# Kernel tuning notes

Measured on AMD Instinct MI355X. Metric: run time of the kernel, lower is better.

Reference implementation:

```python
import jax, jax.numpy as jnp
import numpy as np

D_MODEL = 1024


def pos_encoding(seq_len, d_model):
    # pos: [S,1], i: [d/2]
    pos = jnp.arange(seq_len, dtype=jnp.float32)[:, None]
    i = jnp.arange(0, d_model, 2, dtype=jnp.float32)
    angle_rates = 1.0 / jnp.power(10000.0, i / d_model)
    angle_rads = pos * angle_rates  # [S, d/2]
    # NOTE: original concatenates sin block then cos block (not interleaved)
    return jnp.concatenate([jnp.sin(angle_rads), jnp.cos(angle_rads)], axis=-1)  # [S, d]


def setup_inputs() -> dict:
    key = jax.random.key(0)
    ks = jax.random.split(key, 4)
    B, S, D = 4, 2048, D_MODEL
    scale = 1.0 / np.sqrt(D)
    x = jax.random.normal(ks[0], (B, S, D), dtype=jnp.float32)
    Wq = jax.random.normal(ks[1], (D, D), dtype=jnp.float32) * scale
    Wk = jax.random.normal(ks[2], (D, D), dtype=jnp.float32) * scale
    Wv = jax.random.normal(ks[3], (D, D), dtype=jnp.float32) * scale
    bq = jnp.zeros((D,), dtype=jnp.float32)
    bk = jnp.zeros((D,), dtype=jnp.float32)
    bv = jnp.zeros((D,), dtype=jnp.float32)
    return {"x": x, "Wq": Wq, "bq": bq, "Wk": Wk, "bk": bk, "Wv": Wv, "bv": bv}


def reference(x, Wq, bq, Wk, bk, Wv, bv):
    B, S, D = x.shape
    pe = pos_encoding(S, D)  # [S, D]
    h = x + pe[None, :, :]
    q = jnp.einsum('bsd,de->bse', h, Wq) + bq
    k = jnp.einsum('bsd,de->bse', h, Wk) + bk
    v = jnp.einsum('bsd,de->bse', h, Wv) + bv
    logits = jnp.einsum('bqd,bkd->bqk', q, k) / jnp.sqrt(jnp.float32(D))
    attn = jax.nn.softmax(logits, axis=-1)
    out = jnp.einsum('bqk,bkd->bqd', attn, v)
    return x + out
```

## Files before the change

kernel.cpp:

```cpp
#include <hip/hip_runtime.h>
#include <stdint.h>


#define AS1(p) ((__attribute__((address_space(1))) void*)(p))
#define AS3(p) ((__attribute__((address_space(3))) void*)(p))

typedef _Float16 f16x8 __attribute__((ext_vector_type(8)));
typedef _Float16 f16x4 __attribute__((ext_vector_type(4)));
typedef float f32x4 __attribute__((ext_vector_type(4)));

__global__ __launch_bounds__(256) void prep(const float* __restrict__ x,
                                            _Float16* __restrict__ h,
                                            const float* __restrict__ Wq,
                                            const float* __restrict__ Wk,
                                            const float* __restrict__ Wv,
                                            _Float16* __restrict__ Wt,
                                            float* __restrict__ rowsum) {
  const int bx = blockIdx.x;
  const int tid = threadIdx.x;
  if (bx < 8192) {
    const size_t e = ((size_t)bx * 256 + tid) * 4;
    const int d = (int)(e & 1023);
    const int s = (int)((e >> 10) & 2047);
    const float4 xv = *(const float4*)(x + e);
    const int half = d >> 9;
    const int j0 = d & 511;
    const float c = -0.017988946039016f;
    f16x4 o;
#pragma unroll
    for (int t = 0; t < 4; t++) {
      const float r = __expf((float)(j0 + t) * c);
      const float a = (float)s * r;
      const float p = half ? __cosf(a) : __sinf(a);
      const float xe = (t == 0) ? xv.x : (t == 1) ? xv.y : (t == 2) ? xv.z : xv.w;
      o[t] = (_Float16)(xe + p);
    }
    *(f16x4*)(h + e) = o;
  } else if (bx < 11264) {
    __shared__ float t[32][33];
    const int w = bx - 8192;
    const int z = w >> 10;
    const int rem = w & 1023;
    const int n0 = (rem & 31) * 32, k0 = (rem >> 5) * 32;
    const float* W = (z == 0) ? Wq : (z == 1) ? Wk : Wv;
    _Float16* o = Wt + (size_t)z * 1048576;
    const int tx = tid & 31, ty = tid >> 5;
#pragma unroll
    for (int i = ty; i < 32; i += 8)
      t[i][tx] = W[(size_t)(k0 + i) * 1024 + (n0 + tx)];
    __syncthreads();
#pragma unroll
    for (int i = ty; i < 32; i += 8)
      o[(size_t)(n0 + i) * 1024 + (k0 + tx)] = (_Float16)t[tx][i];
  } else {
    rowsum[(bx - 11264) * 256 + tid] = 0.f;
  }
}

template <int MODE>
__global__ __launch_bounds__(256) void gemm_bt(
    const _Float16* __restrict__ A0, long long sA,
    const _Float16* __restrict__ B0, long long sB,
    void* __restrict__ C0, long long sC,
    const float* __restrict__ aux0, const float* __restrict__ aux1,
    const float* __restrict__ aux2, float* __restrict__ rowsum,
    _Float16* __restrict__ vT,
    long long sX, const int K, const int N, const int ldc) {
  __shared__ __align__(16) _Float16 As[4 * 4096];
  __shared__ __align__(16) _Float16 Bs[4 * 4096];
  const int tid = threadIdx.x;
  const int bid = blockIdx.x;

  int z, bm0, bn0;
  if (MODE == 0) {
    const int c = bid & 7, t = bid >> 3;
    const int mhi = t & 7, u = t >> 3;
    bm0 = (mhi * 8 + c) * 128;
    bn0 = (u & 7) * 128;
    z = u >> 3;
  } else if (MODE == 1) {
    const int c = bid & 7, t = bid >> 3;
    const int zx = (t & 7) * 8 + c;
    const int y = t >> 3;
    z = zx >> 4; bm0 = (zx & 15) * 128; bn0 = y * 128;
  } else {
    const int c = bid & 7, t = bid >> 3;
    const int zx = (t & 3) * 8 + c;
    const int y = t >> 2;
    z = zx >> 3; bm0 = (zx & 7) * 128; bn0 = y * 128;
  }
  const _Float16* A = A0 + (size_t)z * sA;
  const _Float16* Bt = B0 + (size_t)z * sB;

  const _Float16* a0 = A + (size_t)(bm0 + (tid >> 2)) * K + (tid & 3) * 8;
  const _Float16* a1 = a0 + (size_t)64 * K;
  const _Float16* b0 = Bt + (size_t)(bn0 + (tid >> 2)) * K + (tid & 3) * 8;
  const _Float16* b1 = b0 + (size_t)64 * K;

  auto stage = [&](int s) {
    const int r = s & 3;
    const int k = s * 32;
    __builtin_amdgcn_global_load_lds(AS1(a0 + k), AS3(&As[r * 4096 + tid * 8]), 16, 0, 0);
    __builtin_amdgcn_global_load_lds(AS1(a1 + k), AS3(&As[r * 4096 + tid * 8 + 2048]), 16, 0, 0);
    __builtin_amdgcn_global_load_lds(AS1(b0 + k), AS3(&Bs[r * 4096 + tid * 8]), 16, 0, 0);
    __builtin_amdgcn_global_load_lds(AS1(b1 + k), AS3(&Bs[r * 4096 + tid * 8 + 2048]), 16, 0, 0);
  };

  const int lane = tid & 63, wave = tid >> 6;
  const int wr = wave >> 1, wc = wave & 1;
  const int quad = lane >> 4, l16 = lane & 15;

  f32x4 acc[4][4];
#pragma unroll
  for (int i = 0; i < 4; i++)
#pragma unroll
    for (int j = 0; j < 4; j++) {
      f32x4 zz = {0.f, 0.f, 0.f, 0.f};
      acc[i][j] = zz;
    }

  const int NS = K >> 5;

  stage(0); stage(1); stage(2);
  asm volatile("s_waitcnt vmcnt(8)" ::: "memory");
  __builtin_amdgcn_s_barrier();

  for (int s = 0; s < NS; ++s) {
    const int r = s & 3;
    f16x8 af[4], bf[4];
#pragma unroll
    for (int i = 0; i < 4; i++)
      af[i] = *(const f16x8*)&As[r * 4096 + (wr * 64 + i * 16 + l16) * 32 + quad * 8];
#pragma unroll
    for (int j = 0; j < 4; j++)
      bf[j] = *(const f16x8*)&Bs[r * 4096 + (wc * 64 + j * 16 + l16) * 32 + quad * 8];
    if (s + 3 < NS) stage(s + 3);
    __builtin_amdgcn_s_barrier();
    asm volatile("s_waitcnt lgkmcnt(0)" ::: "memory");
    __builtin_amdgcn_sched_barrier(0);
    __builtin_amdgcn_s_setprio(1);
#pragma unroll
    for (int i = 0; i < 4; i++)
#pragma unroll
      for (int j = 0; j < 4; j++)
        acc[i][j] = __builtin_amdgcn_mfma_f32_16x16x32_f16(af[i], bf[j],
                                                           acc[i][j], 0, 0, 0);
    __builtin_amdgcn_s_setprio(0);
    __builtin_amdgcn_sched_barrier(0);
    if (s + 1 < NS) {
      if (s + 3 < NS)       asm volatile("s_waitcnt vmcnt(8)" ::: "memory");
      else if (s + 3 == NS) asm volatile("s_waitcnt vmcnt(4)" ::: "memory");
      else                  asm volatile("s_waitcnt vmcnt(0)" ::: "memory");
      __builtin_amdgcn_s_barrier();
    }
  }

  const int rowb = bm0 + wr * 64 + quad * 4;
  const int colb = bn0 + wc * 64 + l16;
  if (MODE == 0) {
    const float* bias = (z == 0) ? aux0 : (z == 1) ? aux1 : aux2;
    if (z == 2) {
      const int b = rowb >> 11, sl = rowb & 2047;
      _Float16* vb = vT + (size_t)b * 2097152;
#pragma unroll
      for (int i = 0; i < 4; i++)
#pragma unroll
        for (int j = 0; j < 4; j++) {
          const int gn = colb + j * 16;
          const float bb = bias[gn];
          f16x4 o;
#pragma unroll
          for (int r = 0; r < 4; r++) o[r] = (_Float16)(acc[i][j][r] + bb);
          *(f16x4*)&vb[(size_t)gn * 2048 + sl + i * 16] = o;
        }
    } else {
      _Float16* C = (_Float16*)C0 + (size_t)z * sC;
#pragma unroll
      for (int i = 0; i < 4; i++)
#pragma unroll
        for (int j = 0; j < 4; j++) {
          const int gn = colb + j * 16;
          const float bb = bias[gn];
#pragma unroll
          for (int r = 0; r < 4; r++)
            C[(size_t)(rowb + i * 16 + r) * N + gn] = (_Float16)(acc[i][j][r] + bb);
        }
    }
  } else if (MODE == 1) {
    _Float16* C = (_Float16*)C0 + (size_t)z * sC;
    float rs[4] = {0.f, 0.f, 0.f, 0.f};
#pragma unroll
    for (int i = 0; i < 4; i++)
#pragma unroll
      for (int j = 0; j < 4; j++) {
        const int gn = colb + j * 16;
        f16x4 o;
        float pj = 0.f;
#pragma unroll
        for (int r = 0; r < 4; r++) {
          const float e = __expf(acc[i][j][r] * 0.03125f);
          o[r] = (_Float16)e;
          pj += e;
        }
        rs[j] += pj;
        *(f16x4*)&C[(size_t)gn * ldc + rowb + i * 16] = o;
      }
#pragma unroll
    for (int j = 0; j < 4; j++) {
      float v = rs[j];
      v += __shfl_xor(v, 16);
      v += __shfl_xor(v, 32);
      if (quad == 0) atomicAdd(&rowsum[z * 2048 + colb + j * 16], v);
    }
  } else {
    float* C = (float*)C0 + (size_t)z * sC;
    const float* X = aux0 + (size_t)z * sX;
    float inv[4];
#pragma unroll
    for (int j = 0; j < 4; j++)
      inv[j] = 1.0f / rowsum[z * 2048 + colb + j * 16];
#pragma unroll
    for (int i = 0; i < 4; i++)
#pragma unroll
      for (int j = 0; j < 4; j++) {
        const int gn = colb + j * 16;
        const size_t base = (size_t)gn * ldc + rowb + i * 16;
        const float4 xv = *(const float4*)(X + base);
        float4 o;
        o.x = acc[i][j][0] * inv[j] + xv.x;
        o.y = acc[i][j][1] * inv[j] + xv.y;
        o.z = acc[i][j][2] * inv[j] + xv.z;
        o.w = acc[i][j][3] * inv[j] + xv.w;
        *(float4*)(C + base) = o;
      }
  }
}

extern "C" void kernel_launch(void* const* d_in, const int* in_sizes, int n_in,
                              void* d_out, int out_size, void* d_ws, size_t ws_size,
                              hipStream_t stream) {
  (void)in_sizes; (void)n_in; (void)out_size; (void)ws_size;
  const float* x  = (const float*)d_in[0];
  const float* Wq = (const float*)d_in[1];
  const float* bq = (const float*)d_in[2];
  const float* Wk = (const float*)d_in[3];
  const float* bk = (const float*)d_in[4];
  const float* Wv = (const float*)d_in[5];
  const float* bv = (const float*)d_in[6];
  float* out = (float*)d_out;
  char* ws = (char*)d_ws;

  _Float16* h    = (_Float16*)(ws);
  _Float16* Wt   = (_Float16*)(ws + 16777216);
  _Float16* qkv  = (_Float16*)(ws + 23068672);
  _Float16* attn = (_Float16*)(ws + 73400320);
  float* rowsum  = (float*)   (ws + 106954752);

  const long long E = 8388608;
  _Float16* vT = qkv + 2 * E;

  prep<<<11296, 256, 0, stream>>>(x, h, Wq, Wk, Wv, Wt, rowsum);

  gemm_bt<0><<<1536, 256, 0, stream>>>(
      h, 0LL, Wt, 1048576LL, qkv, E, bq, bk, bv, nullptr, vT,
      0LL, 1024, 1024, 0);

  gemm_bt<1><<<1024, 256, 0, stream>>>(
      qkv + E, 2097152LL, qkv, 2097152LL, attn, 4194304LL,
      nullptr, nullptr, nullptr, rowsum, nullptr,
      0LL, 1024, 2048, 2048);

  gemm_bt<2><<<512, 256, 0, stream>>>(
      vT, 2097152LL, attn, 4194304LL, out, 2097152LL,
      x, nullptr, nullptr, rowsum, nullptr,
      2097152LL, 2048, 2048, 1024);
}
```

Before: 266.7 us.

## Deepen GEMM LDS pipeline to five stages with register double-buffered fragments

Raises the shared-memory ring from four to five k-tiles and prefetches four tiles ahead instead of three. LDS fragment reads for the next k-step are issued into a second register set before the MFMAs of the current step, so LDS read latency overlaps with the matrix math. This removes the per-iteration lgkmcnt(0) wait and one barrier. In exchange it uses more LDS, which may lower occupancy, and more VGPRs for the second fragment set, and it relies on the barrier placement to keep the ring slots from being overwritten while still being read.

```diff
diff --git a/kernel.cpp b/kernel.cpp
--- a/kernel.cpp
+++ b/kernel.cpp
@@ -57,6 +57,35 @@
   }
 }
 
+#define READ_FRAGS(r, AF, BF)                                                 \
+  {                                                                           \
+    const int rb_ = (r) * 4096;                                               \
+    _Pragma("unroll") for (int i_ = 0; i_ < 4; i_++)                          \
+      AF[i_] = *(const f16x8*)&As[rb_ + (wr * 64 + i_ * 16 + l16) * 32 + quad * 8]; \
+    _Pragma("unroll") for (int j_ = 0; j_ < 4; j_++)                          \
+      BF[j_] = *(const f16x8*)&Bs[rb_ + (wc * 64 + j_ * 16 + l16) * 32 + quad * 8]; \
+  }
+
+#define DO_MFMA(AF, BF)                                                       \
+  {                                                                           \
+    __builtin_amdgcn_s_setprio(1);                                            \
+    _Pragma("unroll") for (int i_ = 0; i_ < 4; i_++)                          \
+      _Pragma("unroll") for (int j_ = 0; j_ < 4; j_++)                        \
+        acc[i_][j_] = __builtin_amdgcn_mfma_f32_16x16x32_f16(AF[i_], BF[j_],  \
+                                                             acc[i_][j_], 0, 0, 0); \
+    __builtin_amdgcn_s_setprio(0);                                            \
+  }
+
+#define END_PHASE(sv)                                                         \
+  {                                                                           \
+    if ((sv) + 1 < NS) {                                                      \
+      if ((sv) + 5 <= NS)      asm volatile("s_waitcnt vmcnt(8)" ::: "memory"); \
+      else if ((sv) + 4 == NS) asm volatile("s_waitcnt vmcnt(4)" ::: "memory"); \
+      else                     asm volatile("s_waitcnt vmcnt(0)" ::: "memory"); \
+      __builtin_amdgcn_s_barrier();                                           \
+    }                                                                         \
+  }
+
 template <int MODE>
 __global__ __launch_bounds__(256) void gemm_bt(
     const _Float16* __restrict__ A0, long long sA,
@@ -66,8 +95,8 @@
     const float* __restrict__ aux2, float* __restrict__ rowsum,
     _Float16* __restrict__ vT,
     long long sX, const int K, const int N, const int ldc) {
-  __shared__ __align__(16) _Float16 As[4 * 4096];
-  __shared__ __align__(16) _Float16 Bs[4 * 4096];
+  __shared__ __align__(16) _Float16 As[5 * 4096];
+  __shared__ __align__(16) _Float16 Bs[5 * 4096];
   const int tid = threadIdx.x;
   const int bid = blockIdx.x;
 
@@ -97,9 +126,8 @@
   const _Float16* b0 = Bt + (size_t)(bn0 + (tid >> 2)) * K + (tid & 3) * 8;
   const _Float16* b1 = b0 + (size_t)64 * K;
 
-  auto stage = [&](int s) {
-    const int r = s & 3;
-    const int k = s * 32;
+  auto stage = [&](int kt, int r) {
+    const int k = kt * 32;
     __builtin_amdgcn_global_load_lds(AS1(a0 + k), AS3(&As[r * 4096 + tid * 8]), 16, 0, 0);
     __builtin_amdgcn_global_load_lds(AS1(a1 + k), AS3(&As[r * 4096 + tid * 8 + 2048]), 16, 0, 0);
     __builtin_amdgcn_global_load_lds(AS1(b0 + k), AS3(&Bs[r * 4096 + tid * 8]), 16, 0, 0);
@@ -121,37 +149,32 @@
 
   const int NS = K >> 5;
 
-  stage(0); stage(1); stage(2);
+  stage(0, 0); stage(1, 1); stage(2, 2); stage(3, 3);
   asm volatile("s_waitcnt vmcnt(8)" ::: "memory");
   __builtin_amdgcn_s_barrier();
 
-  for (int s = 0; s < NS; ++s) {
-    const int r = s & 3;
-    f16x8 af[4], bf[4];
-#pragma unroll
-    for (int i = 0; i < 4; i++)
-      af[i] = *(const f16x8*)&As[r * 4096 + (wr * 64 + i * 16 + l16) * 32 + quad * 8];
-#pragma unroll
-    for (int j = 0; j < 4; j++)
-      bf[j] = *(const f16x8*)&Bs[r * 4096 + (wc * 64 + j * 16 + l16) * 32 + quad * 8];
-    if (s + 3 < NS) stage(s + 3);
-    __builtin_amdgcn_s_barrier();
-    asm volatile("s_waitcnt lgkmcnt(0)" ::: "memory");
+  f16x8 afA[4], bfA[4], afB[4], bfB[4];
+  READ_FRAGS(0, afA, bfA);
+
+  int rr = 1;
+  int sr = 4;
+
+  for (int s = 0; s < NS; s += 2) {
+    if (s + 1 < NS) { READ_FRAGS(rr, afB, bfB); rr = (rr == 4) ? 0 : rr + 1; }
+    if (s + 4 < NS) { stage(s + 4, sr); sr = (sr == 4) ? 0 : sr + 1; }
     __builtin_amdgcn_sched_barrier(0);
-    __builtin_amdgcn_s_setprio(1);
-#pragma unroll
-    for (int i = 0; i < 4; i++)
-#pragma unroll
-      for (int j = 0; j < 4; j++)
-        acc[i][j] = __builtin_amdgcn_mfma_f32_16x16x32_f16(af[i], bf[j],
-                                                           acc[i][j], 0, 0, 0);
-    __builtin_amdgcn_s_setprio(0);
+    DO_MFMA(afA, bfA);
     __builtin_amdgcn_sched_barrier(0);
-    if (s + 1 < NS) {
-      if (s + 3 < NS)       asm volatile("s_waitcnt vmcnt(8)" ::: "memory");
-      else if (s + 3 == NS) asm volatile("s_waitcnt vmcnt(4)" ::: "memory");
-      else                  asm volatile("s_waitcnt vmcnt(0)" ::: "memory");
-      __builtin_amdgcn_s_barrier();
+    END_PHASE(s);
+
+    const int s1 = s + 1;
+    if (s1 < NS) {
+      if (s1 + 1 < NS) { READ_FRAGS(rr, afA, bfA); rr = (rr == 4) ? 0 : rr + 1; }
+      if (s1 + 4 < NS) { stage(s1 + 4, sr); sr = (sr == 4) ? 0 : sr + 1; }
+      __builtin_amdgcn_sched_barrier(0);
+      DO_MFMA(afB, bfB);
+      __builtin_amdgcn_sched_barrier(0);
+      END_PHASE(s1);
     }
   }
 
```

Measured after the change: 287.1 us. 1.08x slower.
